# Kernel optimization log

Measured on AMD Instinct MI355X. Metric: run time of the kernel, lower is better.

The kernel has to match this reference:

```python
import jax, jax.numpy as jnp
import numpy as np

N_NODES = 50000


def gcn_conv(x, edge_index, W, b):
    """GCNConv with added self-loops and symmetric D^-1/2 (A+I) D^-1/2 normalization."""
    n = x.shape[0]
    h = x @ W  # [N, out]
    loop = jnp.arange(n, dtype=edge_index.dtype)
    src = jnp.concatenate([edge_index[0], loop])
    dst = jnp.concatenate([edge_index[1], loop])
    ones = jnp.ones(src.shape[0], dtype=x.dtype)
    deg = jax.ops.segment_sum(ones, dst, num_segments=n)  # in-degree incl. self-loop
    dis = jnp.where(deg > 0, jax.lax.rsqrt(deg), 0.0).astype(x.dtype)
    norm = dis[src] * dis[dst]  # [E+N]
    msg = h[src] * norm[:, None]  # gather + scale
    out = jax.ops.segment_sum(msg, dst, num_segments=n)  # scatter-add
    return out + b


def setup_inputs() -> dict:
    key = jax.random.key(0)
    ks = jax.random.split(key, 6)
    d_in, d_h, d_out = 256, 256, 128
    x = jax.random.normal(ks[0], (N_NODES, d_in), dtype=jnp.float32)
    edge_index = jax.random.randint(ks[1], (2, 1600000), 0, N_NODES, dtype=jnp.int64)
    edge_label_index = jax.random.randint(ks[2], (2, 100000), 0, N_NODES, dtype=jnp.int64)
    W1 = jax.random.normal(ks[3], (d_in, d_h), dtype=jnp.float32) * (1.0 / np.sqrt(d_in))
    b1 = jnp.zeros((d_h,), dtype=jnp.float32)
    W2 = jax.random.normal(ks[4], (d_h, d_out), dtype=jnp.float32) * (1.0 / np.sqrt(d_h))
    b2 = jnp.zeros((d_out,), dtype=jnp.float32)
    return {"x": x, "edge_index": edge_index, "edge_label_index": edge_label_index,
            "W1": W1, "b1": b1, "W2": W2, "b2": b2}


def reference(x, edge_index, edge_label_index, W1, b1, W2, b2):
    # encode (eval mode: dropout is identity)
    z = jax.nn.relu(gcn_conv(x, edge_index, W1, b1))
    z = gcn_conv(z, edge_index, W2, b2)  # [N, 128]
    # decode: gather endpoint embeddings and reduce (edge dot-product scores)
    y = jnp.sum(z[edge_label_index[0]] * z[edge_label_index[1]], axis=-1)  # [E_label]
    return y
```

## Files before the change

kernel.cpp:

```cpp
#include <hip/hip_runtime.h>
#include <hip/hip_bf16.h>


#define CH 4096

typedef __attribute__((ext_vector_type(8))) short short8;
typedef __attribute__((ext_vector_type(4))) float f32x4;
typedef __attribute__((ext_vector_type(4))) unsigned int u32x4;

__device__ __forceinline__ unsigned short f2bf_rne(float f) {
  unsigned int b = __float_as_uint(f);
  b += 0x7FFFu + ((b >> 16) & 1u);
  return (unsigned short)(b >> 16);
}
__device__ __forceinline__ float bf_lo(unsigned int u) {
  return __uint_as_float(u << 16);
}
__device__ __forceinline__ float bf_hi(unsigned int u) {
  return __uint_as_float(u & 0xFFFF0000u);
}
__device__ __forceinline__ float i8_0(unsigned int r) { return (float)((int)(r << 24) >> 24); }
__device__ __forceinline__ float i8_1(unsigned int r) { return (float)((int)(r << 16) >> 24); }
__device__ __forceinline__ float i8_2(unsigned int r) { return (float)((int)(r << 8) >> 24); }
__device__ __forceinline__ float i8_3(unsigned int r) { return (float)((int)r >> 24); }

__global__ void prep_k(const float* __restrict__ W1, unsigned short* __restrict__ W1t,
                       int K1, int N1, const float* __restrict__ W2,
                       unsigned short* __restrict__ W2t, int K2, int N2) {
  int i = blockIdx.x * blockDim.x + threadIdx.x;
  int m1 = K1 * N1;
  if (i < m1) {
    int k = i / N1, c = i % N1;
    W1t[(size_t)c * K1 + k] = f2bf_rne(W1[i]);
  } else if (i < m1 + K2 * N2) {
    int j2 = i - m1;
    int k = j2 / N2, c = j2 % N2;
    W2t[(size_t)c * K2 + k] = f2bf_rne(W2[j2]);
  }
}

__launch_bounds__(256) __global__
void hist_k(const int* __restrict__ dst, int* __restrict__ cnt, int E, int NB) {
  __shared__ int h[256];
  int t = threadIdx.x, b = blockIdx.x;
  h[t] = 0;
  __syncthreads();
  int i0 = b * CH, i1 = i0 + CH;
  if (i1 > E) i1 = E;
  for (int i = i0 + t; i < i1; i += 256) {
    int d = __builtin_nontemporal_load(&dst[i]);
    atomicAdd(&h[d >> 8], 1);
  }
  __syncthreads();
  cnt[(size_t)t * NB + b] = h[t];
}

__launch_bounds__(256) __global__
void scan1_k(int* __restrict__ cnt, int* __restrict__ tot, int NB) {
  __shared__ int v[1024];
  int t = threadIdx.x, b = blockIdx.x;
  for (int j = t; j < NB; j += 256) v[j] = cnt[(size_t)b * NB + j];
  __syncthreads();
  if (t == 0) {
    int s = 0;
    for (int j = 0; j < NB; j++) { int c = v[j]; v[j] = s; s += c; }
    tot[b] = s;
  }
  __syncthreads();
  for (int j = t; j < NB; j += 256) cnt[(size_t)b * NB + j] = v[j];
}

__global__ void scan2_k(const int* __restrict__ tot, int* __restrict__ bstart) {
  if (threadIdx.x == 0 && blockIdx.x == 0) {
    int s = 0;
    for (int b = 0; b < 256; b++) { bstart[b] = s; s += tot[b]; }
  }
}

__launch_bounds__(256) __global__
void scat_k(const int* __restrict__ src, const int* __restrict__ dst,
            const int* __restrict__ cnt, const int* __restrict__ bstart,
            unsigned int* __restrict__ rec, int E, int NB) {
  __shared__ int ofs[256];
  __shared__ int c2[256];
  int t = threadIdx.x, b = blockIdx.x;
  ofs[t] = bstart[t] + cnt[(size_t)t * NB + b];
  c2[t] = 0;
  __syncthreads();
  int i0 = b * CH, i1 = i0 + CH;
  if (i1 > E) i1 = E;
  for (int i = i0 + t; i < i1; i += 256) {
    int d = __builtin_nontemporal_load(&dst[i]);
    int s = __builtin_nontemporal_load(&src[i]);
    int bk = d >> 8;
    int r = atomicAdd(&c2[bk], 1);
    rec[(size_t)(ofs[bk] + r)] = ((unsigned int)(d & 255) << 16) | (unsigned int)s;
  }
}

__launch_bounds__(256) __global__
void sort2_k(const unsigned int* __restrict__ rec, const int* __restrict__ tot,
             const int* __restrict__ bstart, unsigned short* __restrict__ edges,
             int* __restrict__ rowst, int* __restrict__ fill, int n) {
  __shared__ int hist[256], scanv[256], c2[256];
  int t = threadIdx.x, b = blockIdx.x;
  int nrec = tot[b], bs = bstart[b];
  hist[t] = 0;
  __syncthreads();
  const unsigned int* rp = rec + bs;
  for (int i = t; i < nrec; i += 256) atomicAdd(&hist[rp[i] >> 16], 1);
  __syncthreads();
  if (t == 0) {
    int s = 0;
    for (int k = 0; k < 256; k++) { scanv[k] = s; s += hist[k]; }
  }
  __syncthreads();
  int d = b * 256 + t;
  if (d < n) { fill[d] = hist[t]; rowst[d] = bs + scanv[t]; }
  c2[t] = 0;
  __syncthreads();
  for (int i = t; i < nrec; i += 256) {
    unsigned int r = rp[i];
    int dl = (int)(r >> 16);
    int pos = scanv[dl] + atomicAdd(&c2[dl], 1);
    edges[(size_t)bs + pos] = (unsigned short)r;
  }
}

__global__ void dis_k(const int* __restrict__ fill, float* __restrict__ dis, int n) {
  int i = blockIdx.x * blockDim.x + threadIdx.x;
  if (i < n) dis[i] = rsqrtf((float)(fill[i] + 1));
}

#define LDST 40
template <bool AF32>
__launch_bounds__(256) __global__
void bfgemm_k(const void* __restrict__ Av,
              const unsigned short* __restrict__ Bt,
              unsigned short* __restrict__ C,
              int M, int N, int K) {
  __shared__ short As[128 * LDST];
  __shared__ short Bs[128 * LDST];
  int t = threadIdx.x;
  int lane = t & 63, wave = t >> 6;
  int quad = lane >> 4, l16 = lane & 15;
  int wm = (wave & 1) * 64, wn = (wave >> 1) * 64;
  int m0 = blockIdx.y * 128, n0 = blockIdx.x * 128;
  f32x4 acc[4][4];
#pragma unroll
  for (int i = 0; i < 4; i++)
#pragma unroll
    for (int j = 0; j < 4; j++) acc[i][j] = (f32x4)0.f;

  for (int k0 = 0; k0 < K; k0 += 32) {
    uint4 av[2], bv[2];
#pragma unroll
    for (int u = 0; u < 2; u++) {
      int idx = t + u * 256;
      int row = idx >> 2, c8 = (idx & 3) * 8;
      int gr = m0 + row;
      if (AF32) {
        const float* A = (const float*)Av;
        float4 f0 = make_float4(0.f, 0.f, 0.f, 0.f), f1 = f0;
        if (gr < M) {
          f0 = *reinterpret_cast<const float4*>(A + (size_t)gr * K + k0 + c8);
          f1 = *reinterpret_cast<const float4*>(A + (size_t)gr * K + k0 + c8 + 4);
        }
        av[u].x = (unsigned)f2bf_rne(f0.x) | ((unsigned)f2bf_rne(f0.y) << 16);
        av[u].y = (unsigned)f2bf_rne(f0.z) | ((unsigned)f2bf_rne(f0.w) << 16);
        av[u].z = (unsigned)f2bf_rne(f1.x) | ((unsigned)f2bf_rne(f1.y) << 16);
        av[u].w = (unsigned)f2bf_rne(f1.z) | ((unsigned)f2bf_rne(f1.w) << 16);
      } else {
        const unsigned short* A = (const unsigned short*)Av;
        av[u] = make_uint4(0u, 0u, 0u, 0u);
        if (gr < M)
          av[u] = *reinterpret_cast<const uint4*>(A + (size_t)gr * K + k0 + c8);
      }
      bv[u] = *reinterpret_cast<const uint4*>(Bt + (size_t)(n0 + row) * K + k0 + c8);
    }
    __syncthreads();
#pragma unroll
    for (int u = 0; u < 2; u++) {
      int idx = t + u * 256;
      int row = idx >> 2, c8 = (idx & 3) * 8;
      *reinterpret_cast<uint4*>(&As[row * LDST + c8]) = av[u];
      *reinterpret_cast<uint4*>(&Bs[row * LDST + c8]) = bv[u];
    }
    __syncthreads();
    short8 af[4], bfr[4];
#pragma unroll
    for (int mt = 0; mt < 4; mt++)
      af[mt] = *reinterpret_cast<const short8*>(&As[(wm + mt * 16 + l16) * LDST + quad * 8]);
#pragma unroll
    for (int nt = 0; nt < 4; nt++)
      bfr[nt] = *reinterpret_cast<const short8*>(&Bs[(wn + nt * 16 + l16) * LDST + quad * 8]);
#pragma unroll
    for (int mt = 0; mt < 4; mt++)
#pragma unroll
      for (int nt = 0; nt < 4; nt++)
        acc[mt][nt] = __builtin_amdgcn_mfma_f32_16x16x32_bf16(af[mt], bfr[nt], acc[mt][nt], 0, 0, 0);
  }
#pragma unroll
  for (int mt = 0; mt < 4; mt++) {
#pragma unroll
    for (int r = 0; r < 4; r++) {
      int grow = m0 + wm + mt * 16 + quad * 4 + r;
      if (grow >= M) continue;
      unsigned short* cp = C + (size_t)grow * N + n0 + wn + l16;
#pragma unroll
      for (int nt = 0; nt < 4; nt++) cp[nt * 16] = f2bf_rne(acc[mt][nt][r]);
    }
  }
}

template <int DIM>
__launch_bounds__(256) __global__
void quant_k(const unsigned short* __restrict__ h, const float* __restrict__ dis,
             void* __restrict__ qv, float* __restrict__ ws, int n) {
  const int C = DIM / 64;
  int wave = threadIdx.x >> 6, lane = threadIdx.x & 63;
  int node = blockIdx.x * 4 + wave;
  if (node >= n) return;
  float v[4];
  if (DIM == 256) {
    uint2 r = *reinterpret_cast<const uint2*>(h + (size_t)node * DIM + lane * 4);
    v[0] = bf_lo(r.x); v[1] = bf_hi(r.x); v[2] = bf_lo(r.y); v[3] = bf_hi(r.y);
  } else {
    unsigned int r = *reinterpret_cast<const unsigned int*>(h + (size_t)node * DIM + lane * 2);
    v[0] = bf_lo(r); v[1] = bf_hi(r);
  }
  float amax = 0.f;
#pragma unroll
  for (int i = 0; i < C; i++) amax = fmaxf(amax, fabsf(v[i]));
#pragma unroll
  for (int off = 32; off; off >>= 1) amax = fmaxf(amax, __shfl_xor(amax, off));
  float inv = amax > 0.f ? 127.f / amax : 0.f;
  int q[4];
#pragma unroll
  for (int i = 0; i < C; i++) {
    int t = (int)rintf(v[i] * inv);
    q[i] = t > 127 ? 127 : (t < -127 ? -127 : t);
  }
  if (DIM == 256) {
    unsigned int p = (unsigned int)(q[0] & 255) | ((unsigned int)(q[1] & 255) << 8) |
                     ((unsigned int)(q[2] & 255) << 16) | ((unsigned int)(q[3] & 255) << 24);
    ((unsigned int*)qv)[(size_t)node * 64 + lane] = p;
  } else {
    unsigned short p = (unsigned short)((q[0] & 255) | ((q[1] & 255) << 8));
    ((unsigned short*)qv)[(size_t)node * 64 + lane] = p;
  }
  if (lane == 0) ws[node] = dis[node] * amax * (1.f / 127.f);
}

template <int VEC, bool RELU, bool OBF>
__launch_bounds__(256) __global__
void aggregate_k(const void* __restrict__ qv, const int* __restrict__ fill,
                 const int* __restrict__ rowst, const unsigned short* __restrict__ edges,
                 const float* __restrict__ ws, const float* __restrict__ dis,
                 const float* __restrict__ bias, void* __restrict__ outv, int n) {
  const int DIM = VEC * 64;
  int wave = threadIdx.x >> 6, lane = threadIdx.x & 63;
  int node = blockIdx.x * (blockDim.x >> 6) + wave;
  if (node >= n) return;
  int start = rowst[node], end = start + fill[node];
  float di = dis[node];
  const unsigned int* q4 = (const unsigned int*)qv;
  const unsigned short* q2 = (const unsigned short*)qv;
  float acc[VEC];
  {
    float w = ws[node];
    if (VEC == 4) {
      unsigned int r = q4[(size_t)node * 64 + lane];
      acc[0] = i8_0(r) * w; acc[1] = i8_1(r) * w;
      acc[2] = i8_2(r) * w; acc[3] = i8_3(r) * w;
    } else {
      unsigned int r = q2[(size_t)node * 64 + lane];
      acc[0] = i8_0(r) * w; acc[1] = i8_1(r) * w;
    }
  }
  int e = start;
  for (; e < end && (e & 7); e++) {
    unsigned int s = edges[e];
    float w = ws[s];
    if (VEC == 4) {
      unsigned int r = q4[(size_t)s * 64 + lane];
      acc[0] = fmaf(i8_0(r), w, acc[0]);
      acc[1] = fmaf(i8_1(r), w, acc[1]);
      acc[2] = fmaf(i8_2(r), w, acc[2]);
      acc[3] = fmaf(i8_3(r), w, acc[3]);
    } else {
      unsigned int r = q2[(size_t)s * 64 + lane];
      acc[0] = fmaf(i8_0(r), w, acc[0]);
      acc[1] = fmaf(i8_1(r), w, acc[1]);
    }
  }
  for (; e + 8 <= end; e += 8) {
    u32x4 ev = __builtin_nontemporal_load(reinterpret_cast<const u32x4*>(&edges[e]));
    unsigned int s[8];
    s[0] = ev.x & 0xFFFFu; s[1] = ev.x >> 16;
    s[2] = ev.y & 0xFFFFu; s[3] = ev.y >> 16;
    s[4] = ev.z & 0xFFFFu; s[5] = ev.z >> 16;
    s[6] = ev.w & 0xFFFFu; s[7] = ev.w >> 16;
    float w[8];
#pragma unroll
    for (int j = 0; j < 8; j++) w[j] = ws[s[j]];
    if (VEC == 4) {
      unsigned int r[8];
#pragma unroll
      for (int j = 0; j < 8; j++) r[j] = q4[(size_t)s[j] * 64 + lane];
#pragma unroll
      for (int j = 0; j < 8; j++) {
        acc[0] = fmaf(i8_0(r[j]), w[j], acc[0]);
        acc[1] = fmaf(i8_1(r[j]), w[j], acc[1]);
        acc[2] = fmaf(i8_2(r[j]), w[j], acc[2]);
        acc[3] = fmaf(i8_3(r[j]), w[j], acc[3]);
      }
    } else {
      unsigned int r[8];
#pragma unroll
      for (int j = 0; j < 8; j++) r[j] = q2[(size_t)s[j] * 64 + lane];
#pragma unroll
      for (int j = 0; j < 8; j++) {
        acc[0] = fmaf(i8_0(r[j]), w[j], acc[0]);
        acc[1] = fmaf(i8_1(r[j]), w[j], acc[1]);
      }
    }
  }
  for (; e < end; e++) {
    unsigned int s = edges[e];
    float w = ws[s];
    if (VEC == 4) {
      unsigned int r = q4[(size_t)s * 64 + lane];
      acc[0] = fmaf(i8_0(r), w, acc[0]);
      acc[1] = fmaf(i8_1(r), w, acc[1]);
      acc[2] = fmaf(i8_2(r), w, acc[2]);
      acc[3] = fmaf(i8_3(r), w, acc[3]);
    } else {
      unsigned int r = q2[(size_t)s * 64 + lane];
      acc[0] = fmaf(i8_0(r), w, acc[0]);
      acc[1] = fmaf(i8_1(r), w, acc[1]);
    }
  }
#pragma unroll
  for (int v = 0; v < VEC; v++) {
    float r = fmaf(di, acc[v], bias[lane * VEC + v]);
    if (RELU) r = fmaxf(r, 0.f);
    acc[v] = r;
  }
  if (OBF) {
    unsigned short* op = (unsigned short*)outv + (size_t)node * DIM + lane * VEC;
    if (VEC == 4) {
      unsigned int p0 = (unsigned int)f2bf_rne(acc[0]) | ((unsigned int)f2bf_rne(acc[1]) << 16);
      unsigned int p1 = (unsigned int)f2bf_rne(acc[2]) | ((unsigned int)f2bf_rne(acc[3]) << 16);
      *reinterpret_cast<uint2*>(op) = make_uint2(p0, p1);
    } else {
      unsigned int p0 = (unsigned int)f2bf_rne(acc[0]) | ((unsigned int)f2bf_rne(acc[1]) << 16);
      *reinterpret_cast<unsigned int*>(op) = p0;
    }
  } else {
    float* op = (float*)outv + (size_t)node * DIM + lane * VEC;
#pragma unroll
    for (int v = 0; v < VEC; v++) op[v] = acc[v];
  }
}

__launch_bounds__(256) __global__
void decode_k(const float* __restrict__ z, const int* __restrict__ ea,
              const int* __restrict__ eb, float* __restrict__ y, int E) {
  int wave = threadIdx.x >> 6, lane = threadIdx.x & 63;
  int e = blockIdx.x * (blockDim.x >> 6) + wave;
  if (e >= E) return;
  int a = ea[e], b = eb[e];
  const float2* za = reinterpret_cast<const float2*>(z + (size_t)a * 128);
  const float2* zb = reinterpret_cast<const float2*>(z + (size_t)b * 128);
  float2 pa = za[lane], pb = zb[lane];
  float s = pa.x * pb.x + pa.y * pb.y;
#pragma unroll
  for (int off = 32; off; off >>= 1) s += __shfl_down(s, off);
  if (lane == 0) y[e] = s;
}

extern "C" void kernel_launch(void* const* d_in, const int* in_sizes, int n_in,
                              void* d_out, int out_size, void* d_ws, size_t ws_size,
                              hipStream_t stream) {
  const float* x = (const float*)d_in[0];
  const int* ei = (const int*)d_in[1];
  const int* eli = (const int*)d_in[2];
  const float* W1 = (const float*)d_in[3];
  const float* b1 = (const float*)d_in[4];
  const float* W2 = (const float*)d_in[5];
  const float* b2 = (const float*)d_in[6];
  float* y = (float*)d_out;

  const int DIN = 256, DH = 256, DOUT = 128;
  const int n = in_sizes[0] / DIN;
  const int E = in_sizes[1] / 2;
  const int EL = in_sizes[2] / 2;
  const int* src = ei;
  const int* dst = ei + E;
  const int* ea = eli;
  const int* eb = eli + EL;

  const int NB = (E + CH - 1) / CH;
  const int NBUCK = (n + 255) / 256;

  size_t off = 0;
  auto alloc = [&](size_t bytes) {
    void* p = (char*)d_ws + off;
    off += (bytes + 255) & ~(size_t)255;
    return p;
  };
  int* fill = (int*)alloc((size_t)n * 4);
  int* rowst = (int*)alloc((size_t)n * 4);
  int* cnt = (int*)alloc((size_t)256 * NB * 4);
  int* tot = (int*)alloc((size_t)256 * 4);
  int* bstart = (int*)alloc((size_t)256 * 4);
  unsigned int* rec = (unsigned int*)alloc((size_t)E * 4);
  float* dis = (float*)alloc((size_t)n * 4);
  float* ws = (float*)alloc((size_t)n * 4);
  unsigned short* edges = (unsigned short*)alloc((size_t)E * 2);
  unsigned short* W1t = (unsigned short*)alloc((size_t)DIN * DH * 2);
  unsigned short* W2t = (unsigned short*)alloc((size_t)DH * DOUT * 2);
  unsigned short* h1 = (unsigned short*)alloc((size_t)n * DH * 2);
  unsigned short* z1b = (unsigned short*)alloc((size_t)n * DH * 2);
  unsigned int* qbuf = (unsigned int*)alloc((size_t)n * 64 * 4);
  float* z2 = (float*)h1;
  (void)ws_size;

  prep_k<<<(DIN * DH + DH * DOUT + 255) / 256, 256, 0, stream>>>(W1, W1t, DIN, DH,
                                                                 W2, W2t, DH, DOUT);

  hist_k<<<NB, 256, 0, stream>>>(dst, cnt, E, NB);
  scan1_k<<<256, 256, 0, stream>>>(cnt, tot, NB);
  scan2_k<<<1, 64, 0, stream>>>(tot, bstart);
  scat_k<<<NB, 256, 0, stream>>>(src, dst, cnt, bstart, rec, E, NB);
  sort2_k<<<NBUCK, 256, 0, stream>>>(rec, tot, bstart, edges, rowst, fill, n);
  dis_k<<<(n + 255) / 256, 256, 0, stream>>>(fill, dis, n);

  {
    dim3 grid(DH / 128, (n + 127) / 128);
    bfgemm_k<true><<<grid, 256, 0, stream>>>(x, W1t, h1, n, DH, DIN);
  }
  quant_k<256><<<(n + 3) / 4, 256, 0, stream>>>(h1, dis, qbuf, ws, n);
  aggregate_k<4, true, true><<<(n + 3) / 4, 256, 0, stream>>>(qbuf, fill, rowst, edges,
                                                              ws, dis, b1, z1b, n);

  unsigned short* h2 = h1;
  {
    dim3 grid(DOUT / 128, (n + 127) / 128);
    bfgemm_k<false><<<grid, 256, 0, stream>>>(z1b, W2t, h2, n, DOUT, DH);
  }
  quant_k<128><<<(n + 3) / 4, 256, 0, stream>>>(h2, dis, qbuf, ws, n);
  aggregate_k<2, false, false><<<(n + 3) / 4, 256, 0, stream>>>(qbuf, fill, rowst, edges,
                                                                ws, dis, b2, z2, n);

  decode_k<<<(EL + 3) / 4, 256, 0, stream>>>(z2, ea, eb, y, EL);
}
```

Measured before the change: 398.2 us.

## Fuse int8 quantization into GEMM epilogue and merge small prep kernels

Quantization moves into the GEMM epilogue, so the bf16 intermediate h is never written or re-read. Features are stored in the MFMA output layout, with a permuted bias and a permuted W2 to match. Layer 1 now uses one scale per 128-column half instead of per row. The weight prep is folded into the histogram kernel, scan2 into a per-block shared-memory scan, and dis into the sort kernel, which cuts launches; the layer-2 input permutation adds correctness risk.

```diff
diff --git a/kernel.cpp b/kernel.cpp
--- a/kernel.cpp
+++ b/kernel.cpp
@@ -13,46 +13,44 @@
   b += 0x7FFFu + ((b >> 16) & 1u);
   return (unsigned short)(b >> 16);
 }
-__device__ __forceinline__ float bf_lo(unsigned int u) {
-  return __uint_as_float(u << 16);
-}
-__device__ __forceinline__ float bf_hi(unsigned int u) {
-  return __uint_as_float(u & 0xFFFF0000u);
-}
 __device__ __forceinline__ float i8_0(unsigned int r) { return (float)((int)(r << 24) >> 24); }
 __device__ __forceinline__ float i8_1(unsigned int r) { return (float)((int)(r << 16) >> 24); }
 __device__ __forceinline__ float i8_2(unsigned int r) { return (float)((int)(r << 8) >> 24); }
 __device__ __forceinline__ float i8_3(unsigned int r) { return (float)((int)r >> 24); }
 
-__global__ void prep_k(const float* __restrict__ W1, unsigned short* __restrict__ W1t,
-                       int K1, int N1, const float* __restrict__ W2,
-                       unsigned short* __restrict__ W2t, int K2, int N2) {
-  int i = blockIdx.x * blockDim.x + threadIdx.x;
-  int m1 = K1 * N1;
-  if (i < m1) {
-    int k = i / N1, c = i % N1;
-    W1t[(size_t)c * K1 + k] = f2bf_rne(W1[i]);
-  } else if (i < m1 + K2 * N2) {
-    int j2 = i - m1;
-    int k = j2 / N2, c = j2 % N2;
-    W2t[(size_t)c * K2 + k] = f2bf_rne(W2[j2]);
-  }
-}
-
-__launch_bounds__(256) __global__
-void hist_k(const int* __restrict__ dst, int* __restrict__ cnt, int E, int NB) {
-  __shared__ int h[256];
+__device__ __forceinline__ int dim1_of(int p) {
+  return ((p >> 7) << 7) + (((p >> 6) & 1) << 6) + ((p >> 2) & 15) + ((p & 3) << 4);
+}
+
+__launch_bounds__(256) __global__
+void hist_prep_k(const int* __restrict__ dst, int* __restrict__ cnt, int E, int NB,
+                 const float* __restrict__ W1, unsigned short* __restrict__ W1t,
+                 const float* __restrict__ W2, unsigned short* __restrict__ W2t) {
   int t = threadIdx.x, b = blockIdx.x;
-  h[t] = 0;
-  __syncthreads();
-  int i0 = b * CH, i1 = i0 + CH;
-  if (i1 > E) i1 = E;
-  for (int i = i0 + t; i < i1; i += 256) {
-    int d = __builtin_nontemporal_load(&dst[i]);
-    atomicAdd(&h[d >> 8], 1);
-  }
-  __syncthreads();
-  cnt[(size_t)t * NB + b] = h[t];
+  if (b < NB) {
+    __shared__ int h[256];
+    h[t] = 0;
+    __syncthreads();
+    int i0 = b * CH, i1 = i0 + CH;
+    if (i1 > E) i1 = E;
+    for (int i = i0 + t; i < i1; i += 256) {
+      int d = __builtin_nontemporal_load(&dst[i]);
+      atomicAdd(&h[d >> 8], 1);
+    }
+    __syncthreads();
+    cnt[(size_t)t * NB + b] = h[t];
+    return;
+  }
+  int j = (b - NB) * 256 + t;
+  const int m1 = 256 * 256;
+  if (j < m1) {
+    int k = j >> 8, c = j & 255;
+    W1t[(size_t)c * 256 + k] = f2bf_rne(W1[j]);
+  } else if (j < m1 + 128 * 256) {
+    int j2 = j - m1;
+    int c = j2 >> 8, p = j2 & 255;
+    W2t[(size_t)c * 256 + p] = f2bf_rne(W2[(size_t)dim1_of(p) * 128 + c]);
+  }
 }
 
 __launch_bounds__(256) __global__
@@ -70,21 +68,28 @@
   for (int j = t; j < NB; j += 256) cnt[(size_t)b * NB + j] = v[j];
 }
 
-__global__ void scan2_k(const int* __restrict__ tot, int* __restrict__ bstart) {
-  if (threadIdx.x == 0 && blockIdx.x == 0) {
-    int s = 0;
-    for (int b = 0; b < 256; b++) { bstart[b] = s; s += tot[b]; }
+__device__ __forceinline__ void scan256(const int* __restrict__ tot, int* bl, int t) {
+  bl[t] = tot[t];
+  __syncthreads();
+#pragma unroll
+  for (int s2 = 1; s2 < 256; s2 <<= 1) {
+    int v = (t >= s2) ? bl[t - s2] : 0;
+    __syncthreads();
+    bl[t] += v;
+    __syncthreads();
   }
 }
 
 __launch_bounds__(256) __global__
 void scat_k(const int* __restrict__ src, const int* __restrict__ dst,
-            const int* __restrict__ cnt, const int* __restrict__ bstart,
+            const int* __restrict__ cnt, const int* __restrict__ tot,
             unsigned int* __restrict__ rec, int E, int NB) {
+  __shared__ int bl[256];
   __shared__ int ofs[256];
   __shared__ int c2[256];
   int t = threadIdx.x, b = blockIdx.x;
-  ofs[t] = bstart[t] + cnt[(size_t)t * NB + b];
+  scan256(tot, bl, t);
+  ofs[t] = (bl[t] - tot[t]) + cnt[(size_t)t * NB + b];
   c2[t] = 0;
   __syncthreads();
   int i0 = b * CH, i1 = i0 + CH;
@@ -99,12 +104,14 @@
 }
 
 __launch_bounds__(256) __global__
-void sort2_k(const unsigned int* __restrict__ rec, const int* __restrict__ tot,
-             const int* __restrict__ bstart, unsigned short* __restrict__ edges,
-             int* __restrict__ rowst, int* __restrict__ fill, int n) {
-  __shared__ int hist[256], scanv[256], c2[256];
+void sort2_dis_k(const unsigned int* __restrict__ rec, const int* __restrict__ tot,
+                 unsigned short* __restrict__ edges, int* __restrict__ rowst,
+                 int* __restrict__ fill, float* __restrict__ dis, int n) {
+  __shared__ int bl[256], hist[256], scanv[256], c2[256];
   int t = threadIdx.x, b = blockIdx.x;
-  int nrec = tot[b], bs = bstart[b];
+  int nrec = tot[b];
+  scan256(tot, bl, t);
+  int bs = bl[b] - nrec;
   hist[t] = 0;
   __syncthreads();
   const unsigned int* rp = rec + bs;
@@ -116,7 +123,11 @@
   }
   __syncthreads();
   int d = b * 256 + t;
-  if (d < n) { fill[d] = hist[t]; rowst[d] = bs + scanv[t]; }
+  if (d < n) {
+    fill[d] = hist[t];
+    rowst[d] = bs + scanv[t];
+    dis[d] = rsqrtf((float)(hist[t] + 1));
+  }
   c2[t] = 0;
   __syncthreads();
   for (int i = t; i < nrec; i += 256) {
@@ -127,24 +138,23 @@
   }
 }
 
-__global__ void dis_k(const int* __restrict__ fill, float* __restrict__ dis, int n) {
-  int i = blockIdx.x * blockDim.x + threadIdx.x;
-  if (i < n) dis[i] = rsqrtf((float)(fill[i] + 1));
-}
-
 #define LDST 40
-template <bool AF32>
-__launch_bounds__(256) __global__
-void bfgemm_k(const void* __restrict__ Av,
-              const unsigned short* __restrict__ Bt,
-              unsigned short* __restrict__ C,
-              int M, int N, int K) {
+template <bool AF32, int QROWW>
+__launch_bounds__(256) __global__
+void gemmq_k(const void* __restrict__ Av,
+             const unsigned short* __restrict__ Bt,
+             unsigned int* __restrict__ Q,
+             float* __restrict__ wsout,
+             const float* __restrict__ dis,
+             int M, int N, int K) {
   __shared__ short As[128 * LDST];
   __shared__ short Bs[128 * LDST];
+  __shared__ float rm[128][2];
   int t = threadIdx.x;
   int lane = t & 63, wave = t >> 6;
   int quad = lane >> 4, l16 = lane & 15;
   int wm = (wave & 1) * 64, wn = (wave >> 1) * 64;
+  int wn6 = wn >> 6;
   int m0 = blockIdx.y * 128, n0 = blockIdx.x * 128;
   f32x4 acc[4][4];
 #pragma unroll
@@ -200,59 +210,48 @@
       for (int nt = 0; nt < 4; nt++)
         acc[mt][nt] = __builtin_amdgcn_mfma_f32_16x16x32_bf16(af[mt], bfr[nt], acc[mt][nt], 0, 0, 0);
   }
+
 #pragma unroll
   for (int mt = 0; mt < 4; mt++) {
 #pragma unroll
     for (int r = 0; r < 4; r++) {
-      int grow = m0 + wm + mt * 16 + quad * 4 + r;
+      float m = fmaxf(fmaxf(fabsf(acc[mt][0][r]), fabsf(acc[mt][1][r])),
+                      fmaxf(fabsf(acc[mt][2][r]), fabsf(acc[mt][3][r])));
+#pragma unroll
+      for (int off = 1; off < 16; off <<= 1) m = fmaxf(m, __shfl_xor(m, off));
+      if (l16 == 0) rm[wm + mt * 16 + quad * 4 + r][wn6] = m;
+    }
+  }
+  __syncthreads();
+#pragma unroll
+  for (int mt = 0; mt < 4; mt++) {
+#pragma unroll
+    for (int r = 0; r < 4; r++) {
+      int rl = wm + mt * 16 + quad * 4 + r;
+      int grow = m0 + rl;
       if (grow >= M) continue;
-      unsigned short* cp = C + (size_t)grow * N + n0 + wn + l16;
-#pragma unroll
-      for (int nt = 0; nt < 4; nt++) cp[nt * 16] = f2bf_rne(acc[mt][nt][r]);
-    }
-  }
-}
-
-template <int DIM>
-__launch_bounds__(256) __global__
-void quant_k(const unsigned short* __restrict__ h, const float* __restrict__ dis,
-             void* __restrict__ qv, float* __restrict__ ws, int n) {
-  const int C = DIM / 64;
-  int wave = threadIdx.x >> 6, lane = threadIdx.x & 63;
-  int node = blockIdx.x * 4 + wave;
-  if (node >= n) return;
-  float v[4];
-  if (DIM == 256) {
-    uint2 r = *reinterpret_cast<const uint2*>(h + (size_t)node * DIM + lane * 4);
-    v[0] = bf_lo(r.x); v[1] = bf_hi(r.x); v[2] = bf_lo(r.y); v[3] = bf_hi(r.y);
-  } else {
-    unsigned int r = *reinterpret_cast<const unsigned int*>(h + (size_t)node * DIM + lane * 2);
-    v[0] = bf_lo(r); v[1] = bf_hi(r);
-  }
-  float amax = 0.f;
-#pragma unroll
-  for (int i = 0; i < C; i++) amax = fmaxf(amax, fabsf(v[i]));
-#pragma unroll
-  for (int off = 32; off; off >>= 1) amax = fmaxf(amax, __shfl_xor(amax, off));
-  float inv = amax > 0.f ? 127.f / amax : 0.f;
-  int q[4];
-#pragma unroll
-  for (int i = 0; i < C; i++) {
-    int t = (int)rintf(v[i] * inv);
-    q[i] = t > 127 ? 127 : (t < -127 ? -127 : t);
-  }
-  if (DIM == 256) {
-    unsigned int p = (unsigned int)(q[0] & 255) | ((unsigned int)(q[1] & 255) << 8) |
-                     ((unsigned int)(q[2] & 255) << 16) | ((unsigned int)(q[3] & 255) << 24);
-    ((unsigned int*)qv)[(size_t)node * 64 + lane] = p;
-  } else {
-    unsigned short p = (unsigned short)((q[0] & 255) | ((q[1] & 255) << 8));
-    ((unsigned short*)qv)[(size_t)node * 64 + lane] = p;
-  }
-  if (lane == 0) ws[node] = dis[node] * amax * (1.f / 127.f);
-}
-
-template <int VEC, bool RELU, bool OBF>
+      float mx = fmaxf(rm[rl][0], rm[rl][1]);
+      float inv = mx > 0.f ? 127.f / mx : 0.f;
+      int qv[4];
+#pragma unroll
+      for (int nt = 0; nt < 4; nt++) {
+        int tq = (int)rintf(acc[mt][nt][r] * inv);
+        qv[nt] = tq > 127 ? 127 : (tq < -127 ? -127 : tq);
+      }
+      unsigned int pk = (unsigned)(qv[0] & 255) | ((unsigned)(qv[1] & 255) << 8) |
+                        ((unsigned)(qv[2] & 255) << 16) | ((unsigned)(qv[3] & 255) << 24);
+      int qcol = (QROWW == 64 ? (n0 >> 7) * 32 : 0) + wn6 * 16 + l16;
+      Q[(size_t)grow * QROWW + qcol] = pk;
+      if (wn6 == 0 && l16 == 0) {
+        float sc = dis[grow] * mx * (1.f / 127.f);
+        if (QROWW == 64) wsout[grow * 2 + (n0 >> 7)] = sc;
+        else wsout[grow] = sc;
+      }
+    }
+  }
+}
+
+template <int VEC, bool RELU, bool OBF, bool WS2>
 __launch_bounds__(256) __global__
 void aggregate_k(const void* __restrict__ qv, const int* __restrict__ fill,
                  const int* __restrict__ rowst, const unsigned short* __restrict__ edges,
@@ -264,11 +263,22 @@
   if (node >= n) return;
   int start = rowst[node], end = start + fill[node];
   float di = dis[node];
+  int hsel = lane >> 5;
+  float bv[VEC];
+  if (VEC == 4) {
+    int base = (hsel << 7) + (((lane >> 4) & 1) << 6) + (lane & 15);
+#pragma unroll
+    for (int v = 0; v < 4; v++) bv[v] = bias[base + (v << 4)];
+  } else {
+    int c0 = (hsel << 6) + ((lane >> 1) & 15) + ((lane & 1) << 5);
+    bv[0] = bias[c0];
+    bv[1] = bias[c0 + 16];
+  }
   const unsigned int* q4 = (const unsigned int*)qv;
   const unsigned short* q2 = (const unsigned short*)qv;
   float acc[VEC];
   {
-    float w = ws[node];
+    float w = WS2 ? ws[2 * node + hsel] : ws[node];
     if (VEC == 4) {
       unsigned int r = q4[(size_t)node * 64 + lane];
       acc[0] = i8_0(r) * w; acc[1] = i8_1(r) * w;
@@ -281,7 +291,7 @@
   int e = start;
   for (; e < end && (e & 7); e++) {
     unsigned int s = edges[e];
-    float w = ws[s];
+    float w = WS2 ? ws[2 * s + hsel] : ws[s];
     if (VEC == 4) {
       unsigned int r = q4[(size_t)s * 64 + lane];
       acc[0] = fmaf(i8_0(r), w, acc[0]);
@@ -303,7 +313,7 @@
     s[6] = ev.w & 0xFFFFu; s[7] = ev.w >> 16;
     float w[8];
 #pragma unroll
-    for (int j = 0; j < 8; j++) w[j] = ws[s[j]];
+    for (int j = 0; j < 8; j++) w[j] = WS2 ? ws[2 * s[j] + hsel] : ws[s[j]];
     if (VEC == 4) {
       unsigned int r[8];
 #pragma unroll
@@ -328,7 +338,7 @@
   }
   for (; e < end; e++) {
     unsigned int s = edges[e];
-    float w = ws[s];
+    float w = WS2 ? ws[2 * s + hsel] : ws[s];
     if (VEC == 4) {
       unsigned int r = q4[(size_t)s * 64 + lane];
       acc[0] = fmaf(i8_0(r), w, acc[0]);
@@ -343,7 +353,7 @@
   }
 #pragma unroll
   for (int v = 0; v < VEC; v++) {
-    float r = fmaf(di, acc[v], bias[lane * VEC + v]);
+    float r = fmaf(di, acc[v], bv[v]);
     if (RELU) r = fmaxf(r, 0.f);
     acc[v] = r;
   }
@@ -403,6 +413,8 @@
 
   const int NB = (E + CH - 1) / CH;
   const int NBUCK = (n + 255) / 256;
+  const int PB = (DIN * DH + DH * DOUT + 255) / 256;
+  const int MB = (n + 127) / 128;
 
   size_t off = 0;
   auto alloc = [&](size_t bytes) {
@@ -414,45 +426,30 @@
   int* rowst = (int*)alloc((size_t)n * 4);
   int* cnt = (int*)alloc((size_t)256 * NB * 4);
   int* tot = (int*)alloc((size_t)256 * 4);
-  int* bstart = (int*)alloc((size_t)256 * 4);
   unsigned int* rec = (unsigned int*)alloc((size_t)E * 4);
   float* dis = (float*)alloc((size_t)n * 4);
-  float* ws = (float*)alloc((size_t)n * 4);
+  float* ws2 = (float*)alloc((size_t)n * 2 * 4);
+  float* wsB = (float*)alloc((size_t)n * 4);
   unsigned short* edges = (unsigned short*)alloc((size_t)E * 2);
   unsigned short* W1t = (unsigned short*)alloc((size_t)DIN * DH * 2);
   unsigned short* W2t = (unsigned short*)alloc((size_t)DH * DOUT * 2);
-  unsigned short* h1 = (unsigned short*)alloc((size_t)n * DH * 2);
+  unsigned int* qbuf = (unsigned int*)alloc((size_t)n * 64 * 4);
   unsigned short* z1b = (unsigned short*)alloc((size_t)n * DH * 2);
-  unsigned int* qbuf = (unsigned int*)alloc((size_t)n * 64 * 4);
-  float* z2 = (float*)h1;
+  float* z2 = (float*)alloc((size_t)n * DOUT * 4);
   (void)ws_size;
 
-  prep_k<<<(DIN * DH + DH * DOUT + 255) / 256, 256, 0, stream>>>(W1, W1t, DIN, DH,
-                                                                 W2, W2t, DH, DOUT);
-
-  hist_k<<<NB, 256, 0, stream>>>(dst, cnt, E, NB);
+  hist_prep_k<<<NB + PB, 256, 0, stream>>>(dst, cnt, E, NB, W1, W1t, W2, W2t);
   scan1_k<<<256, 256, 0, stream>>>(cnt, tot, NB);
-  scan2_k<<<1, 64, 0, stream>>>(tot, bstart);
-  scat_k<<<NB, 256, 0, stream>>>(src, dst, cnt, bstart, rec, E, NB);
-  sort2_k<<<NBUCK, 256, 0, stream>>>(rec, tot, bstart, edges, rowst, fill, n);
-  dis_k<<<(n + 255) / 256, 256, 0, stream>>>(fill, dis, n);
-
-  {
-    dim3 grid(DH / 128, (n + 127) / 128);
-    bfgemm_k<true><<<grid, 256, 0, stream>>>(x, W1t, h1, n, DH, DIN);
-  }
-  quant_k<256><<<(n + 3) / 4, 256, 0, stream>>>(h1, dis, qbuf, ws, n);
-  aggregate_k<4, true, true><<<(n + 3) / 4, 256, 0, stream>>>(qbuf, fill, rowst, edges,
-                                                              ws, dis, b1, z1b, n);
-
-  unsigned short* h2 = h1;
-  {
-    dim3 grid(DOUT / 128, (n + 127) / 128);
-    bfgemm_k<false><<<grid, 256, 0, stream>>>(z1b, W2t, h2, n, DOUT, DH);
-  }
-  quant_k<128><<<(n + 3) / 4, 256, 0, stream>>>(h2, dis, qbuf, ws, n);
-  aggregate_k<2, false, false><<<(n + 3) / 4, 256, 0, stream>>>(qbuf, fill, rowst, edges,
-                                                                ws, dis, b2, z2, n);
+  scat_k<<<NB, 256, 0, stream>>>(src, dst, cnt, tot, rec, E, NB);
+  sort2_dis_k<<<NBUCK, 256, 0, stream>>>(rec, tot, edges, rowst, fill, dis, n);
+
+  gemmq_k<true, 64><<<dim3(2, MB), 256, 0, stream>>>(x, W1t, qbuf, ws2, dis, n, DH, DIN);
+  aggregate_k<4, true, true, true><<<(n + 3) / 4, 256, 0, stream>>>(
+      qbuf, fill, rowst, edges, ws2, dis, b1, z1b, n);
+
+  gemmq_k<false, 32><<<dim3(1, MB), 256, 0, stream>>>(z1b, W2t, qbuf, wsB, dis, n, DOUT, DH);
+  aggregate_k<2, false, false, false><<<(n + 3) / 4, 256, 0, stream>>>(
+      qbuf, fill, rowst, edges, wsB, dis, b2, z2, n);
 
   decode_k<<<(EL + 3) / 4, 256, 0, stream>>>(z2, ea, eb, y, EL);
 }
```

After: 384.7 us. 3.4% less time.
